# Kernel optimization log

Measured on AMD Instinct MI355X. Metric: run time of the kernel, lower is better.

The kernel has to match this reference:

```python
import jax, jax.numpy as jnp
import numpy as np

B, D, H = 16384, 1024, 4096


def setup_inputs() -> dict:
    key = jax.random.key(0)
    kx, kp, k1, k2 = jax.random.split(key, 4)
    X = jax.random.normal(kx, (B, D), dtype=jnp.float32)
    prot_col_idx = 3
    # protected column must be binary {0,1} so the remap produces no NaNs
    prot = jax.random.randint(kp, (B,), 0, 2).astype(jnp.float32)
    X = X.at[:, prot_col_idx].set(prot)
    W1 = jax.random.normal(k1, (D, H), dtype=jnp.float32) * (1.0 / np.sqrt(D))
    b1 = jnp.zeros((H,), dtype=jnp.float32)
    W2 = jax.random.normal(k2, (H, D), dtype=jnp.float32) * (1.0 / np.sqrt(H))
    b2 = jnp.zeros((D,), dtype=jnp.float32)
    return {"X": X, "W1": W1, "b1": b1, "W2": W2, "b2": b2,
            "prot_col_idx": prot_col_idx}


def reference(X, W1, b1, W2, b2, prot_col_idx):
    def explainer(x):
        h = jnp.tanh(x @ W1 + b1)          # [B, H]
        return h @ W2 + b2                  # [B, D]

    # vectorized remap of the protected column: 0 -> 1, 1 -> 0, else NaN
    col = X[:, prot_col_idx]
    flipped = jnp.where(col == 0, jnp.float32(1.0),
                        jnp.where(col == 1, jnp.float32(0.0), jnp.float32(jnp.nan)))
    X_copy = X.at[:, prot_col_idx].set(flipped.astype(X.dtype))

    shaps = explainer(X)
    shaps_counter = explainer(X_copy)
    mean_euclid_dist = jnp.mean(jnp.abs(shaps - shaps_counter), axis=0)  # [D]
    return mean_euclid_dist.sum()
```

## Files before the change

### kernel.cpp

```cpp
#include <hip/hip_runtime.h>
#include <stdint.h>

#define B_N 16384
#define D_N 1024
#define H_N 4096

typedef int i32x4 __attribute__((ext_vector_type(4)));
typedef int i32x8 __attribute__((ext_vector_type(8)));
typedef float f32x4 __attribute__((ext_vector_type(4)));

__device__ __forceinline__ void gload16(const void* g, void* l) {
  __builtin_amdgcn_global_load_lds((const __attribute__((address_space(1))) void*)g,
                                   (__attribute__((address_space(3))) void*)l,
                                   16, 0, 0);
}

__device__ __forceinline__ unsigned char f2fp8(float v) {
  return (unsigned char)(__builtin_amdgcn_cvt_pk_fp8_f32(v, v, 0, false) & 0xFF);
}

__device__ __forceinline__ int perm_h(int h) {
  return (h & ~63) | ((h & 15) << 2) | ((h >> 4) & 3);
}

__device__ __forceinline__ void transpose_tile(
    const float* __restrict__ in, unsigned char* __restrict__ out,
    int R, int C, float scale, float* __restrict__ w3, int pci,
    int i0, int j0, int tx, int ty, bool permute) {
  __shared__ float tile[32][33];
#pragma unroll
  for (int r = 0; r < 32; r += 8) {
    int i = i0 + ty + r;
    int j = j0 + tx;
    float v = in[(size_t)i * C + j];
    tile[ty + r][tx] = v;
    if (w3 != nullptr && i == pci) w3[j] = v;
  }
  __syncthreads();
#pragma unroll
  for (int r = 0; r < 32; r += 8) {
    int jo = j0 + ty + r;
    int io = i0 + tx;
    int ioo = permute ? perm_h(io) : io;
    out[(size_t)jo * R + ioo] = f2fp8(tile[tx][ty + r] * scale);
  }
}

__global__ __launch_bounds__(256) void prep_kernel(
    const float4* __restrict__ X4, int* __restrict__ Xb,
    float* __restrict__ s,
    const float* __restrict__ W1, unsigned char* __restrict__ W1T, float* __restrict__ w3,
    const float* __restrict__ W2, unsigned char* __restrict__ W2T,
    const int* __restrict__ pci_p, float* __restrict__ out0) {
  int b = blockIdx.x;
  int tid = threadIdx.x;
  int pci = *pci_p;
  if (b == 0 && tid == 0) out0[0] = 0.0f;
  if (b < 8192) {
    int i = (b * 256 + tid) * 2;
#pragma unroll
    for (int u = 0; u < 2; u++) {
      float4 v = X4[i + u];
      int p = __builtin_amdgcn_cvt_pk_fp8_f32(v.x, v.y, 0, false);
      p = __builtin_amdgcn_cvt_pk_fp8_f32(v.z, v.w, p, true);
      Xb[i + u] = p;
      if (((i + u) & (D_N / 4 - 1)) == (pci >> 2)) {
        int row = (i + u) >> 8;
        float c;
        switch (pci & 3) {
          case 0:  c = v.x; break;
          case 1:  c = v.y; break;
          case 2:  c = v.z; break;
          default: c = v.w; break;
        }
        s[row] = 1.0f - 2.0f * c;
      }
    }
  } else if (b < 12288) {
    int id = b - 8192;
    transpose_tile(W1, W1T, D_N, H_N, 16.0f, w3, pci,
                   (id >> 7) * 32, (id & 127) * 32, tid & 31, tid >> 5, false);
  } else {
    int id = b - 12288;
    transpose_tile(W2, W2T, H_N, D_N, 64.0f, nullptr, -1,
                   (id >> 5) * 32, (id & 31) * 32, tid & 31, tid >> 5, true);
  }
}

template <int KTOT>
__device__ __forceinline__ void mx_mainloop(
    const unsigned char* __restrict__ A, const unsigned char* __restrict__ B,
    int m0, int n0, int sa, int sb,
    unsigned char* As, unsigned char* Bs, f32x4 (&acc)[4][4]) {
  const int tid = threadIdx.x;
  const int lane = tid & 63;
  const int wave = tid >> 6;
  const int wm = (wave >> 1) * 64;
  const int wn = (wave & 1) * 64;
  const int lm = lane & 15;
  const int quad = lane >> 4;

  const int srow = tid >> 3;
  const int clog = (tid & 7) ^ (srow & 7);
  const unsigned char* Ag = A + (size_t)(m0 + srow) * KTOT + clog * 16;
  const unsigned char* Bg = B + (size_t)(n0 + srow) * KTOT + clog * 16;
  unsigned char* As_l = As + tid * 16;
  unsigned char* Bs_l = Bs + tid * 16;

  for (int k0 = 0; k0 < KTOT; k0 += 128) {
#pragma unroll
    for (int it = 0; it < 4; it++) {
      gload16(Ag + k0 + (size_t)(32 * it) * KTOT, As_l + it * 4096);
      gload16(Bg + k0 + (size_t)(32 * it) * KTOT, Bs_l + it * 4096);
    }
    __syncthreads();
    i32x8 b[4];
#pragma unroll
    for (int j = 0; j < 4; j++) {
      int r = wn + j * 16 + lm;
      int e = r & 7;
      i32x4 lo = *(const i32x4*)&Bs[r * 128 + ((2 * quad) ^ e) * 16];
      i32x4 hi = *(const i32x4*)&Bs[r * 128 + ((2 * quad + 1) ^ e) * 16];
      b[j] = __builtin_shufflevector(lo, hi, 0, 1, 2, 3, 4, 5, 6, 7);
    }
#pragma unroll
    for (int i = 0; i < 4; i++) {
      int r = wm + i * 16 + lm;
      int e = r & 7;
      i32x4 lo = *(const i32x4*)&As[r * 128 + ((2 * quad) ^ e) * 16];
      i32x4 hi = *(const i32x4*)&As[r * 128 + ((2 * quad + 1) ^ e) * 16];
      i32x8 av = __builtin_shufflevector(lo, hi, 0, 1, 2, 3, 4, 5, 6, 7);
#pragma unroll
      for (int j = 0; j < 4; j++)
        acc[i][j] = __builtin_amdgcn_mfma_scale_f32_16x16x128_f8f6f4(
            av, b[j], acc[i][j], 0, 0, 0, sa, 0, sb);
    }
    __syncthreads();
  }
}

__global__ __launch_bounds__(256, 4) void gemm1_dh(
    const unsigned char* __restrict__ Xb,
    const unsigned char* __restrict__ W1T,
    const float* __restrict__ b1,
    const float* __restrict__ w3,
    const float* __restrict__ s,
    unsigned int* __restrict__ Dh4) {
  __shared__ alignas(16) unsigned char As[128 * 128];
  __shared__ alignas(16) unsigned char Bs[128 * 128];
  int l = blockIdx.y * gridDim.x + blockIdx.x;
  int x = l & 7;
  int k = l >> 3;
  int ni = k & 7;
  int m  = (k >> 3) & 15;
  int nc = k >> 7;
  const int m0 = (x * 16 + m) * 128;
  const int n0 = (nc * 8 + ni) * 128;

  f32x4 acc[4][4] = {};
  mx_mainloop<D_N>(Xb, W1T, m0, n0, 127, 123, As, Bs, acc);

  const int tid = threadIdx.x;
  const int lane = tid & 63;
  const int wave = tid >> 6;
  const int wm = (wave >> 1) * 64;
  const int wn = (wave & 1) * 64;
  const int lm = lane & 15;
  const int quad = lane >> 4;

  float ewp[4], ewm[4], nump[4], numm[4], b1v[4];
#pragma unroll
  for (int j = 0; j < 4; j++) {
    int gh = n0 + wn + j * 16 + lm;
    float w = w3[gh];
    float ep = __expf(2.0f * w);
    float em = __expf(-2.0f * w);
    ewp[j] = ep; ewm[j] = em;
    nump[j] = 128.0f * (1.0f - ep);
    numm[j] = 128.0f * (1.0f - em);
    b1v[j] = b1[gh];
  }
  const size_t coloff = (size_t)((n0 + wn) >> 2) + lm;
#pragma unroll
  for (int i = 0; i < 4; i++) {
#pragma unroll
    for (int r = 0; r < 4; r++) {
      int gb = m0 + wm + i * 16 + quad * 4 + r;
      bool sp = s[gb] > 0.0f;
      float o[4];
#pragma unroll
      for (int j = 0; j < 4; j++) {
        float ews = sp ? ewp[j] : ewm[j];
        float num = sp ? nump[j] : numm[j];
        float z = fminf(acc[i][j][r] + b1v[j], 12.0f);
        float E = __expf(2.0f * z);
        float den = (E * ews + 1.0f) * (E + 1.0f);
        o[j] = (E * num) * __builtin_amdgcn_rcpf(den);
      }
      int p = __builtin_amdgcn_cvt_pk_fp8_f32(o[0], o[1], 0, false);
      p = __builtin_amdgcn_cvt_pk_fp8_f32(o[2], o[3], p, true);
      Dh4[(size_t)gb * (H_N / 4) + coloff] = (unsigned int)p;
    }
  }
}

template <int KTOT>
__device__ __forceinline__ void mx8_mainloop(
    const unsigned char* __restrict__ A, const unsigned char* __restrict__ B,
    int m0, int n0, int sa, int sb,
    unsigned char* __restrict__ As, unsigned char* __restrict__ Bs,
    f32x4 (&acc)[8][4]) {
  static_assert(KTOT % 256 == 0, "need an even number of 128-K tiles");
  const int tid = threadIdx.x;
  const int lane = tid & 63;
  const int wave = tid >> 6;
  const int wm = (wave >> 2) * 128;
  const int wn = (wave & 3) * 64;
  const int lm = lane & 15;
  const int quad = lane >> 4;

  const int srow = tid >> 3;
  const int sg = tid & 7;
  const unsigned char* Ag = A + (size_t)(m0 + srow) * KTOT + ((sg ^ (srow & 7)) * 16);
  const unsigned char* Bg = B + (size_t)(n0 + srow) * KTOT + ((sg ^ (srow & 7)) * 16);
  unsigned char* AsW = As + tid * 16;
  unsigned char* BsW = Bs + tid * 16;

  const int e = lm & 7;
  const int lo_off = ((2 * quad) ^ e) * 16;
  const int hi_off = ((2 * quad + 1) ^ e) * 16;
  const unsigned char* Ard_lo = As + (wm + lm) * 128 + lo_off;
  const unsigned char* Ard_hi = As + (wm + lm) * 128 + hi_off;
  const unsigned char* Brd_lo = Bs + (wn + lm) * 128 + lo_off;
  const unsigned char* Brd_hi = Bs + (wn + lm) * 128 + hi_off;

  i32x8 bA0, bA1, bA2, bA3, bB0, bB1, bB2, bB3;
  i32x8 ax0, ax1, ay0, ay1;

#define STGA(c_, kn_, p_) \
    gload16(Ag + (kn_) + (size_t)(c_) * 64 * KTOT, AsW + (p_) * 32768 + (c_) * 8192)
#define STGB(c_, kn_, p_) \
    gload16(Bg + (kn_) + (size_t)(c_) * 64 * KTOT, BsW + (p_) * 32768 + (c_) * 8192)
#define LDA(d_, i_, P_) { \
    i32x4 lo_ = *(const i32x4*)(Ard_lo + (P_) * 32768 + (i_) * 2048); \
    i32x4 hi_ = *(const i32x4*)(Ard_hi + (P_) * 32768 + (i_) * 2048); \
    d_ = __builtin_shufflevector(lo_, hi_, 0, 1, 2, 3, 4, 5, 6, 7); }
#define LDB(d_, j_, P_) { \
    i32x4 lo_ = *(const i32x4*)(Brd_lo + (P_) * 32768 + (j_) * 2048); \
    i32x4 hi_ = *(const i32x4*)(Brd_hi + (P_) * 32768 + (j_) * 2048); \
    d_ = __builtin_shufflevector(lo_, hi_, 0, 1, 2, 3, 4, 5, 6, 7); }
#define MF(a_, b_, c_) \
    __builtin_amdgcn_mfma_scale_f32_16x16x128_f8f6f4((a_), (b_), (c_), 0, 0, 0, sa, 0, sb)
#define BARR() { asm volatile("" ::: "memory"); __builtin_amdgcn_s_barrier(); \
                 asm volatile("" ::: "memory"); }
#define VM(n_) asm volatile("s_waitcnt vmcnt(" #n_ ")" ::: "memory")
#define SCHED0() __builtin_amdgcn_sched_barrier(0)
#define MM8(i0_, i1_, aA_, aB_, B0_, B1_, B2_, B3_) { \
    __builtin_amdgcn_s_setprio(1); \
    acc[i0_][0] = MF(aA_, B0_, acc[i0_][0]); \
    acc[i0_][1] = MF(aA_, B1_, acc[i0_][1]); \
    acc[i0_][2] = MF(aA_, B2_, acc[i0_][2]); \
    acc[i0_][3] = MF(aA_, B3_, acc[i0_][3]); \
    acc[i1_][0] = MF(aB_, B0_, acc[i1_][0]); \
    acc[i1_][1] = MF(aB_, B1_, acc[i1_][1]); \
    acc[i1_][2] = MF(aB_, B2_, acc[i1_][2]); \
    acc[i1_][3] = MF(aB_, B3_, acc[i1_][3]); \
    __builtin_amdgcn_s_setprio(0); }

#define TILE(P_, BC0_, BC1_, BC2_, BC3_, BN0_, BN1_, BN2_, BN3_, kn_, LAST_) { \
    LDA(ay0, 2, P_); LDA(ay1, 3, P_); \
    if (!(LAST_)) { STGB(0, kn_, 1 - (P_)); STGB(1, kn_, 1 - (P_)); } \
    SCHED0(); \
    MM8(0, 1, ax0, ax1, BC0_, BC1_, BC2_, BC3_); \
    if (LAST_) { VM(0); } else { VM(2); } \
    BARR(); \
    LDA(ax0, 4, P_); LDA(ax1, 5, P_); \
    if (!(LAST_)) { STGB(2, kn_, 1 - (P_)); STGB(3, kn_, 1 - (P_)); \
                    STGA(0, kn_, 1 - (P_)); STGA(2, kn_, 1 - (P_)); } \
    SCHED0(); \
    MM8(2, 3, ay0, ay1, BC0_, BC1_, BC2_, BC3_); \
    BARR(); \
    LDA(ay0, 6, P_); LDA(ay1, 7, P_); \
    if (!(LAST_)) { STGA(1, kn_, 1 - (P_)); STGA(3, kn_, 1 - (P_)); } \
    SCHED0(); \
    MM8(4, 5, ax0, ax1, BC0_, BC1_, BC2_, BC3_); \
    if (!(LAST_)) { VM(2); } \
    BARR(); \
    if (!(LAST_)) { \
      LDB(BN0_, 0, 1 - (P_)); LDB(BN1_, 1, 1 - (P_)); \
      LDB(BN2_, 2, 1 - (P_)); LDB(BN3_, 3, 1 - (P_)); \
      LDA(ax0, 0, 1 - (P_)); LDA(ax1, 1, 1 - (P_)); \
    } \
    SCHED0(); \
    MM8(6, 7, ay0, ay1, BC0_, BC1_, BC2_, BC3_); \
    if (!(LAST_)) { BARR(); } \
  }

  STGB(0, 0, 0); STGB(1, 0, 0); STGB(2, 0, 0); STGB(3, 0, 0);
  STGA(0, 0, 0); STGA(2, 0, 0);
  STGA(1, 0, 0); STGA(3, 0, 0);
  VM(2);
  BARR();
  LDB(bA0, 0, 0); LDB(bA1, 1, 0); LDB(bA2, 2, 0); LDB(bA3, 3, 0);
  LDA(ax0, 0, 0); LDA(ax1, 1, 0);

  const int NT = KTOT / 128;
  for (int t = 0; t < NT - 2; t += 2) {
    TILE(0, bA0, bA1, bA2, bA3, bB0, bB1, bB2, bB3, (t + 1) * 128, false);
    TILE(1, bB0, bB1, bB2, bB3, bA0, bA1, bA2, bA3, (t + 2) * 128, false);
  }
  TILE(0, bA0, bA1, bA2, bA3, bB0, bB1, bB2, bB3, (NT - 1) * 128, false);
  TILE(1, bB0, bB1, bB2, bB3, bA0, bA1, bA2, bA3, 0, true);

#undef STGA
#undef STGB
#undef LDA
#undef LDB
#undef MF
#undef BARR
#undef VM
#undef SCHED0
#undef MM8
#undef TILE
}

__global__ __launch_bounds__(512, 2) void gemm2_abs(
    const unsigned char* __restrict__ Dh,
    const unsigned char* __restrict__ W2T,
    float* __restrict__ out) {
  __shared__ alignas(16) unsigned char As[65536];
  __shared__ alignas(16) unsigned char Bs[65536];
  __shared__ float wsum[8];
  const int l = blockIdx.x;
  const int x = l & 7;
  const int k = l >> 3;
  const int m0 = (x * 8 + (k & 7)) * 256;
  const int n0 = (k >> 3) * 256;

  f32x4 acc[8][4] = {};
  mx8_mainloop<H_N>(Dh, W2T, m0, n0, 121, 121, As, Bs, acc);

  const int tid = threadIdx.x;
  const int lane = tid & 63;
  const int wave = tid >> 6;

  float t = 0.0f;
#pragma unroll
  for (int i = 0; i < 8; i++)
#pragma unroll
    for (int j = 0; j < 4; j++)
#pragma unroll
      for (int r = 0; r < 4; r++)
        t += fabsf(acc[i][j][r]);

#pragma unroll
  for (int off2 = 32; off2 > 0; off2 >>= 1)
    t += __shfl_down(t, off2, 64);
  if (lane == 0) wsum[wave] = t;
  __syncthreads();
  if (tid == 0) {
    float tt = 0.0f;
#pragma unroll
    for (int w = 0; w < 8; w++) tt += wsum[w];
    atomicAdd(out, tt * (1.0f / (float)B_N));
  }
}

extern "C" void kernel_launch(void* const* d_in, const int* in_sizes, int n_in,
                              void* d_out, int out_size, void* d_ws, size_t ws_size,
                              hipStream_t stream) {
  const float* X  = (const float*)d_in[0];
  const float* W1 = (const float*)d_in[1];
  const float* b1 = (const float*)d_in[2];
  const float* W2 = (const float*)d_in[3];
  const int* pci  = (const int*)d_in[5];

  char* ws = (char*)d_ws;
  size_t off = 0;
  unsigned char* Xb  = (unsigned char*)(ws + off); off += (size_t)B_N * D_N;
  unsigned char* W1T = (unsigned char*)(ws + off); off += (size_t)H_N * D_N;
  unsigned char* W2T = (unsigned char*)(ws + off); off += (size_t)D_N * H_N;
  float* w3  = (float*)(ws + off); off += (size_t)H_N * 4;
  float* s   = (float*)(ws + off); off += (size_t)B_N * 4;
  unsigned char* Dh  = (unsigned char*)(ws + off); off += (size_t)B_N * H_N;
  if (ws_size < off) return;

  prep_kernel<<<16384, 256, 0, stream>>>((const float4*)X, (int*)Xb, s,
                                         W1, W1T, w3, W2, W2T, pci,
                                         (float*)d_out);
  gemm1_dh<<<dim3(32, 128), 256, 0, stream>>>(Xb, W1T, b1, w3, s,
                                              (unsigned int*)Dh);
  gemm2_abs<<<256, 512, 0, stream>>>(Dh, W2T, (float*)d_out);
}
```

Before: 276.1 us.

## Use two waves per 128x128 tile in gemm1 with 64x128 per-wave subtiles

Cuts the gemm1 block from four waves (each computing a 64x64 subtile) to two waves (each computing 64 rows by all 128 columns). Each wave now does 32 MFMAs per K-step against 8 B-fragment loads, which raises register-level reuse and reduces LDS read traffic per MFMA. Shared-memory address arithmetic is hoisted out of the K loop. In exchange each block has half the threads, so each thread issues twice as many global-to-LDS loads, register pressure doubles for accumulators, and there are fewer waves per CU to hide latency. The epilogue writes two packed fp8 words per row.

```diff
diff --git a/kernel.cpp b/kernel.cpp
--- a/kernel.cpp
+++ b/kernel.cpp
@@ -88,15 +88,14 @@
 }
 
 template <int KTOT>
-__device__ __forceinline__ void mx_mainloop(
+__device__ __forceinline__ void mx_w2_mainloop(
     const unsigned char* __restrict__ A, const unsigned char* __restrict__ B,
     int m0, int n0, int sa, int sb,
-    unsigned char* As, unsigned char* Bs, f32x4 (&acc)[4][4]) {
+    unsigned char* As, unsigned char* Bs, f32x4 (&acc)[4][8]) {
   const int tid = threadIdx.x;
   const int lane = tid & 63;
   const int wave = tid >> 6;
-  const int wm = (wave >> 1) * 64;
-  const int wn = (wave & 1) * 64;
+  const int wm = wave * 64;
   const int lm = lane & 15;
   const int quad = lane >> 4;
 
@@ -107,39 +106,41 @@
   unsigned char* As_l = As + tid * 16;
   unsigned char* Bs_l = Bs + tid * 16;
 
+  const int e = lm & 7;
+  const unsigned char* Ard_lo = As + (wm + lm) * 128 + (((2 * quad) ^ e) * 16);
+  const unsigned char* Ard_hi = As + (wm + lm) * 128 + (((2 * quad + 1) ^ e) * 16);
+  const unsigned char* Brd_lo = Bs + lm * 128 + (((2 * quad) ^ e) * 16);
+  const unsigned char* Brd_hi = Bs + lm * 128 + (((2 * quad + 1) ^ e) * 16);
+
   for (int k0 = 0; k0 < KTOT; k0 += 128) {
 #pragma unroll
-    for (int it = 0; it < 4; it++) {
-      gload16(Ag + k0 + (size_t)(32 * it) * KTOT, As_l + it * 4096);
-      gload16(Bg + k0 + (size_t)(32 * it) * KTOT, Bs_l + it * 4096);
+    for (int it = 0; it < 8; it++) {
+      gload16(Ag + k0 + (size_t)(16 * it) * KTOT, As_l + it * 2048);
+      gload16(Bg + k0 + (size_t)(16 * it) * KTOT, Bs_l + it * 2048);
     }
     __syncthreads();
-    i32x8 b[4];
-#pragma unroll
-    for (int j = 0; j < 4; j++) {
-      int r = wn + j * 16 + lm;
-      int e = r & 7;
-      i32x4 lo = *(const i32x4*)&Bs[r * 128 + ((2 * quad) ^ e) * 16];
-      i32x4 hi = *(const i32x4*)&Bs[r * 128 + ((2 * quad + 1) ^ e) * 16];
-      b[j] = __builtin_shufflevector(lo, hi, 0, 1, 2, 3, 4, 5, 6, 7);
-    }
+    i32x8 a[4];
 #pragma unroll
     for (int i = 0; i < 4; i++) {
-      int r = wm + i * 16 + lm;
-      int e = r & 7;
-      i32x4 lo = *(const i32x4*)&As[r * 128 + ((2 * quad) ^ e) * 16];
-      i32x4 hi = *(const i32x4*)&As[r * 128 + ((2 * quad + 1) ^ e) * 16];
-      i32x8 av = __builtin_shufflevector(lo, hi, 0, 1, 2, 3, 4, 5, 6, 7);
-#pragma unroll
-      for (int j = 0; j < 4; j++)
+      i32x4 lo = *(const i32x4*)(Ard_lo + i * 2048);
+      i32x4 hi = *(const i32x4*)(Ard_hi + i * 2048);
+      a[i] = __builtin_shufflevector(lo, hi, 0, 1, 2, 3, 4, 5, 6, 7);
+    }
+#pragma unroll
+    for (int j = 0; j < 8; j++) {
+      i32x4 lo = *(const i32x4*)(Brd_lo + j * 2048);
+      i32x4 hi = *(const i32x4*)(Brd_hi + j * 2048);
+      i32x8 b = __builtin_shufflevector(lo, hi, 0, 1, 2, 3, 4, 5, 6, 7);
+#pragma unroll
+      for (int i = 0; i < 4; i++)
         acc[i][j] = __builtin_amdgcn_mfma_scale_f32_16x16x128_f8f6f4(
-            av, b[j], acc[i][j], 0, 0, 0, sa, 0, sb);
+            a[i], b, acc[i][j], 0, 0, 0, sa, 0, sb);
     }
     __syncthreads();
   }
 }
 
-__global__ __launch_bounds__(256, 4) void gemm1_dh(
+__global__ __launch_bounds__(128, 2) void gemm1_dh(
     const unsigned char* __restrict__ Xb,
     const unsigned char* __restrict__ W1T,
     const float* __restrict__ b1,
@@ -157,21 +158,20 @@
   const int m0 = (x * 16 + m) * 128;
   const int n0 = (nc * 8 + ni) * 128;
 
-  f32x4 acc[4][4] = {};
-  mx_mainloop<D_N>(Xb, W1T, m0, n0, 127, 123, As, Bs, acc);
+  f32x4 acc[4][8] = {};
+  mx_w2_mainloop<D_N>(Xb, W1T, m0, n0, 127, 123, As, Bs, acc);
 
   const int tid = threadIdx.x;
   const int lane = tid & 63;
   const int wave = tid >> 6;
-  const int wm = (wave >> 1) * 64;
-  const int wn = (wave & 1) * 64;
+  const int wm = wave * 64;
   const int lm = lane & 15;
   const int quad = lane >> 4;
 
-  float ewp[4], ewm[4], nump[4], numm[4], b1v[4];
-#pragma unroll
-  for (int j = 0; j < 4; j++) {
-    int gh = n0 + wn + j * 16 + lm;
+  float ewp[8], ewm[8], nump[8], numm[8], b1v[8];
+#pragma unroll
+  for (int j = 0; j < 8; j++) {
+    int gh = n0 + j * 16 + lm;
     float w = w3[gh];
     float ep = __expf(2.0f * w);
     float em = __expf(-2.0f * w);
@@ -180,16 +180,16 @@
     numm[j] = 128.0f * (1.0f - em);
     b1v[j] = b1[gh];
   }
-  const size_t coloff = (size_t)((n0 + wn) >> 2) + lm;
+  const size_t col0 = (size_t)(n0 >> 2) + lm;
 #pragma unroll
   for (int i = 0; i < 4; i++) {
 #pragma unroll
     for (int r = 0; r < 4; r++) {
       int gb = m0 + wm + i * 16 + quad * 4 + r;
       bool sp = s[gb] > 0.0f;
-      float o[4];
-#pragma unroll
-      for (int j = 0; j < 4; j++) {
+      float o[8];
+#pragma unroll
+      for (int j = 0; j < 8; j++) {
         float ews = sp ? ewp[j] : ewm[j];
         float num = sp ? nump[j] : numm[j];
         float z = fminf(acc[i][j][r] + b1v[j], 12.0f);
@@ -197,9 +197,12 @@
         float den = (E * ews + 1.0f) * (E + 1.0f);
         o[j] = (E * num) * __builtin_amdgcn_rcpf(den);
       }
-      int p = __builtin_amdgcn_cvt_pk_fp8_f32(o[0], o[1], 0, false);
-      p = __builtin_amdgcn_cvt_pk_fp8_f32(o[2], o[3], p, true);
-      Dh4[(size_t)gb * (H_N / 4) + coloff] = (unsigned int)p;
+      int p0 = __builtin_amdgcn_cvt_pk_fp8_f32(o[0], o[1], 0, false);
+      p0 = __builtin_amdgcn_cvt_pk_fp8_f32(o[2], o[3], p0, true);
+      int p1 = __builtin_amdgcn_cvt_pk_fp8_f32(o[4], o[5], 0, false);
+      p1 = __builtin_amdgcn_cvt_pk_fp8_f32(o[6], o[7], p1, true);
+      Dh4[(size_t)gb * (H_N / 4) + col0] = (unsigned int)p0;
+      Dh4[(size_t)gb * (H_N / 4) + col0 + 16] = (unsigned int)p1;
     }
   }
 }
@@ -388,7 +391,7 @@
   prep_kernel<<<16384, 256, 0, stream>>>((const float4*)X, (int*)Xb, s,
                                          W1, W1T, w3, W2, W2T, pci,
                                          (float*)d_out);
-  gemm1_dh<<<dim3(32, 128), 256, 0, stream>>>(Xb, W1T, b1, w3, s,
+  gemm1_dh<<<dim3(32, 128), 128, 0, stream>>>(Xb, W1T, b1, w3, s,
                                               (unsigned int*)Dh);
   gemm2_abs<<<256, 512, 0, stream>>>(Dh, W2T, (float*)d_out);
 }
```

After: 273.2 us. No clear change (-1.1%).
